# Kernel tuning notes

Measured on AMD Instinct MI355X. Metric: run time of the kernel, lower is better.

## Reference

```python
import jax, jax.numpy as jnp
import numpy as np

N, DIM = 20000, 2
E2, E3 = 150000, 100000
H = 512
IN_PAIR = 2 * DIM + 2    # arity*dim + arity (sigma repeated per object)
IN_TRIPLE = 3 * DIM + 3


def _lin(k, fan_in, fan_out):
    return jax.random.normal(k, (fan_in, fan_out), jnp.float32) / np.sqrt(fan_in)


def setup_inputs() -> dict:
    key = jax.random.key(0)
    ks = jax.random.split(key, 18)
    inp = {
        "x": jax.random.normal(ks[0], (N, DIM), jnp.float32),
        "sigma": jax.random.uniform(ks[1], (1,), jnp.float32) + 0.1,
        "edges_pair": jax.random.randint(ks[2], (E2, 2), 0, N),
        "edges_triple": jax.random.randint(ks[3], (E3, 3), 0, N),
        # per-relation-type TimeInputEnergyMLP params (2 hidden layers + scalar head)
        "pW1": _lin(ks[4], IN_PAIR, H), "pb1": jnp.zeros((H,), jnp.float32),
        "pW2": _lin(ks[5], H, H),       "pb2": jnp.zeros((H,), jnp.float32),
        "pW3": _lin(ks[6], H, 1),       "pb3": jnp.zeros((1,), jnp.float32),
        "tW1": _lin(ks[7], IN_TRIPLE, H), "tb1": jnp.zeros((H,), jnp.float32),
        "tW2": _lin(ks[8], H, H),         "tb2": jnp.zeros((H,), jnp.float32),
        "tW3": _lin(ks[9], H, 1),         "tb3": jnp.zeros((1,), jnp.float32),
    }
    return inp


def _mlp_energy(h, W1, b1, W2, b2, W3, b3):
    # h: (E, in_dim) -> (E, 1) scalar energy per edge
    h = jax.nn.silu(h @ W1 + b1)
    h = jax.nn.silu(h @ W2 + b2)
    return h @ W3 + b3


def reference(x, sigma, edges_pair, edges_triple,
              pW1, pb1, pW2, pb2, pW3, pb3,
              tW1, tb1, tW2, tb2, tW3, tb3):
    def total_energy(xx):
        # pair edges: gather -> (E2, 2*DIM), sigma repeated per object -> (E2, 2)
        xp = xx[edges_pair].reshape(edges_pair.shape[0], -1)
        sp = jnp.broadcast_to(sigma, (edges_pair.shape[0], 2))
        ep = _mlp_energy(jnp.concatenate([xp, sp], axis=-1),
                         pW1, pb1, pW2, pb2, pW3, pb3).sum()
        # triple edges
        xt = xx[edges_triple].reshape(edges_triple.shape[0], -1)
        st = jnp.broadcast_to(sigma, (edges_triple.shape[0], 3))
        et = _mlp_energy(jnp.concatenate([xt, st], axis=-1),
                         tW1, tb1, tW2, tb2, tW3, tb3).sum()
        return ep + et

    energy, grad = jax.value_and_grad(total_energy)(x)
    return energy, grad
```

## Files before the change

### kernel.cpp

```cpp
#include <hip/hip_runtime.h>
#include <hip/hip_bf16.h>

#define HDIM 512
#define TILE 64
#define TPB 512

typedef __attribute__((ext_vector_type(8))) short short8;
typedef __attribute__((ext_vector_type(4))) short s16x4;
typedef __attribute__((ext_vector_type(4))) float f32x4;

__device__ __forceinline__ unsigned short f2bf(float x) {
  __hip_bfloat16 h = __float2bfloat16(x);
  return *reinterpret_cast<unsigned short*>(&h);
}
__device__ __forceinline__ float bf2f(unsigned short h) {
  return __uint_as_float(((unsigned)h) << 16);
}
__device__ __forceinline__ float fsig(float z) {
  return __builtin_amdgcn_rcpf(1.f + __expf(-z));
}
__device__ __forceinline__ int bidx(int e, int n) {
  return e * HDIM + (n ^ ((e & 7) << 4));
}

__global__ void prep_weights(const float* __restrict__ pW2, const float* __restrict__ tW2,
                             unsigned short* __restrict__ pWf, unsigned short* __restrict__ pWb,
                             unsigned short* __restrict__ tWf, unsigned short* __restrict__ tWb) {
  int i = blockIdx.x * blockDim.x + threadIdx.x;
  if (i >= HDIM * HDIM) return;
  int j  = i & 7;
  int l  = (i >> 3) & 63;
  int kb = (i >> 9) & 15;
  int nb = i >> 13;
  int kpos = kb * 32 + ((l >> 4) << 3) + j;
  int npos = nb * 16 + (l & 15);
  pWf[i] = f2bf(pW2[kpos * HDIM + npos]);
  pWb[i] = f2bf(pW2[npos * HDIM + kpos]);
  tWf[i] = f2bf(tW2[kpos * HDIM + npos]);
  tWb[i] = f2bf(tW2[npos * HDIM + kpos]);
}

__global__ void prep_w1(const float* __restrict__ W1, int IN, int GD,
                        unsigned short* __restrict__ hi, unsigned short* __restrict__ lo,
                        unsigned short* __restrict__ p5) {
  int i = blockIdx.x * blockDim.x + threadIdx.x;
  if (i < 32 * 64 * 8) {
    int j = i & 7, l = (i >> 3) & 63, nb = i >> 9;
    int k = ((l >> 4) << 3) + j;
    int col = nb * 16 + (l & 15);
    float v = (k < IN) ? W1[k * HDIM + col] : 0.f;
    unsigned short h = f2bf(v);
    hi[i] = h;
    lo[i] = f2bf(v - bf2f(h));
  } else if (i < 32 * 64 * 8 + 16 * 64 * 8) {
    int i2 = i - 32 * 64 * 8;
    int j = i2 & 7, l = (i2 >> 3) & 63, kk = i2 >> 9;
    int lm = l & 15, q = l >> 4;
    int k = kk * 32 + q * 8 + j;
    p5[i2] = f2bf((lm < GD) ? W1[lm * HDIM + k] : 0.f);
  }
}

__global__ void __launch_bounds__(TPB, 2)
energy_kernel(const float* __restrict__ x, const float* __restrict__ sigp,
              const int* __restrict__ ep, const int* __restrict__ et,
              int E2, int E3, int nb2,
              const unsigned short* __restrict__ pW1hi, const unsigned short* __restrict__ pW1lo,
              const unsigned short* __restrict__ pW1p5,
              const unsigned short* __restrict__ tW1hi, const unsigned short* __restrict__ tW1lo,
              const unsigned short* __restrict__ tW1p5,
              const float* __restrict__ pb1, const float* __restrict__ tb1,
              const unsigned short* __restrict__ pWf, const unsigned short* __restrict__ pWb,
              const unsigned short* __restrict__ tWf, const unsigned short* __restrict__ tWb,
              const float* __restrict__ pb2, const float* __restrict__ tb2,
              const float* __restrict__ pw3, const float* __restrict__ tw3,
              const float* __restrict__ pb3, const float* __restrict__ tb3,
              float* __restrict__ out) {
  __shared__ __align__(16) unsigned short bufA[TILE * HDIM];
  __shared__ __align__(16) float h0s[TILE][16];
  __shared__ float dh0sT[8][TILE];
  __shared__ int   idxs[TILE * 3];
  __shared__ float blockE;

  const bool isP = (int)blockIdx.x < nb2;
  const int arity = isP ? 2 : 3;
  const int GD = 2 * arity;
  const int Etot = isP ? E2 : E3;
  const int* __restrict__ edges = isP ? ep : et;
  const unsigned short* __restrict__ W1hi = isP ? pW1hi : tW1hi;
  const unsigned short* __restrict__ W1lo = isP ? pW1lo : tW1lo;
  const unsigned short* __restrict__ W1p5 = isP ? pW1p5 : tW1p5;
  const unsigned short* __restrict__ Wf = isP ? pWf : tWf;
  const unsigned short* __restrict__ Wb = isP ? pWb : tWb;
  const float* __restrict__ b1 = isP ? pb1 : tb1;
  const float* __restrict__ b2 = isP ? pb2 : tb2;
  const float* __restrict__ w3 = isP ? pw3 : tw3;
  const float* __restrict__ b3p = isP ? pb3 : tb3;

  const int tid  = threadIdx.x;
  const int lane = tid & 63;
  const int w    = tid >> 6;
  const int q    = lane >> 4;
  const int lm   = lane & 15;
  const int tile0 = (isP ? (int)blockIdx.x : (int)blockIdx.x - nb2) * TILE;
  const int vcnt  = min(TILE, Etot - tile0);
  const float sigma = sigp[0];

  if (tid == 0) blockE = 0.f;
  ((float*)dh0sT)[tid] = 0.f;
  if (tid < TILE * arity) {
    int e = tid / arity;
    idxs[tid] = (e < vcnt) ? edges[(size_t)tile0 * arity + tid] : 0;
  }
  __syncthreads();
  if (tid < TILE) {
#pragma unroll
    for (int k = 0; k < 16; ++k) h0s[tid][k] = 0.f;
    if (tid < vcnt) {
      for (int o = 0; o < arity; ++o) {
        int id = idxs[tid * arity + o];
        h0s[tid][o * 2 + 0] = x[id * 2 + 0];
        h0s[tid][o * 2 + 1] = x[id * 2 + 1];
        h0s[tid][arity * 2 + o] = sigma;
      }
    }
  }
  __syncthreads();

  const int n0 = w * 64;

  short8 Hh[4], Hl[4];
#pragma unroll
  for (int ef = 0; ef < 4; ++ef) {
    f32x4 v0 = {0.f, 0.f, 0.f, 0.f}, v1 = {0.f, 0.f, 0.f, 0.f};
    if (q < 2) {
      const float* p = &h0s[ef * 16 + lm][q * 8];
      v0 = *(const f32x4*)p;
      v1 = *(const f32x4*)(p + 4);
    }
#pragma unroll
    for (int j = 0; j < 4; ++j) {
      unsigned short ha = f2bf(v0[j]);
      Hh[ef][j] = (short)ha;
      Hl[ef][j] = (short)f2bf(v0[j] - bf2f(ha));
      unsigned short hb = f2bf(v1[j]);
      Hh[ef][j + 4] = (short)hb;
      Hl[ef][j + 4] = (short)f2bf(v1[j] - bf2f(hb));
    }
  }

  f32x4 acc[4][4];
#pragma unroll
  for (int mf = 0; mf < 4; ++mf)
#pragma unroll
    for (int ef = 0; ef < 4; ++ef) acc[mf][ef] = (f32x4){0.f, 0.f, 0.f, 0.f};

#pragma unroll
  for (int mf = 0; mf < 4; ++mf) {
    short8 A1h = *(const short8*)(W1hi + (((w * 4 + mf) * 64 + lane) << 3));
    short8 A1l = *(const short8*)(W1lo + (((w * 4 + mf) * 64 + lane) << 3));
#pragma unroll
    for (int ef = 0; ef < 4; ++ef) {
      acc[mf][ef] = __builtin_amdgcn_mfma_f32_16x16x32_bf16(A1h, Hh[ef], acc[mf][ef], 0, 0, 0);
      acc[mf][ef] = __builtin_amdgcn_mfma_f32_16x16x32_bf16(A1l, Hh[ef], acc[mf][ef], 0, 0, 0);
      acc[mf][ef] = __builtin_amdgcn_mfma_f32_16x16x32_bf16(A1h, Hl[ef], acc[mf][ef], 0, 0, 0);
    }
  }
#pragma unroll
  for (int mf = 0; mf < 4; ++mf) {
    f32x4 b1x = *(const f32x4*)&b1[n0 + mf * 16 + q * 4];
#pragma unroll
    for (int ef = 0; ef < 4; ++ef) {
      bool val = (ef * 16 + lm) < vcnt;
      s16x4 pk;
#pragma unroll
      for (int r = 0; r < 4; ++r) {
        float z = acc[mf][ef][r] + b1x[r];
        float s = fsig(z);
        pk[r] = (short)f2bf(val ? z * s : 0.f);
      }
      *(s16x4*)&bufA[bidx(ef * 16 + lm, n0 + mf * 16 + q * 4)] = pk;
    }
  }
  __syncthreads();

#pragma unroll
  for (int mf = 0; mf < 4; ++mf)
#pragma unroll
    for (int ef = 0; ef < 4; ++ef) acc[mf][ef] = (f32x4){0.f, 0.f, 0.f, 0.f};

  {
    short8 af_cur[4];
#pragma unroll
    for (int mf = 0; mf < 4; ++mf)
      af_cur[mf] = *(const short8*)(Wf + ((((w * 4 + mf) * 16 + 0) * 64 + lane) << 3));
#pragma unroll
    for (int kk = 0; kk < 16; ++kk) {
      short8 af_nxt[4];
      if (kk < 15) {
#pragma unroll
        for (int mf = 0; mf < 4; ++mf)
          af_nxt[mf] = *(const short8*)(Wf + ((((w * 4 + mf) * 16 + kk + 1) * 64 + lane) << 3));
      }
      short8 hb[4];
#pragma unroll
      for (int ef = 0; ef < 4; ++ef)
        hb[ef] = *(const short8*)&bufA[bidx(ef * 16 + lm, kk * 32 + q * 8)];
      __builtin_amdgcn_s_setprio(1);
#pragma unroll
      for (int mf = 0; mf < 4; ++mf)
#pragma unroll
        for (int ef = 0; ef < 4; ++ef)
          acc[mf][ef] = __builtin_amdgcn_mfma_f32_16x16x32_bf16(af_cur[mf], hb[ef], acc[mf][ef], 0, 0, 0);
      __builtin_amdgcn_s_setprio(0);
#pragma unroll
      for (int mf = 0; mf < 4; ++mf) af_cur[mf] = af_nxt[mf];
    }
  }

  float epart = 0.f;
#pragma unroll
  for (int mf = 0; mf < 4; ++mf) {
    f32x4 b2x = *(const f32x4*)&b2[n0 + mf * 16 + q * 4];
    f32x4 w3x = *(const f32x4*)&w3[n0 + mf * 16 + q * 4];
#pragma unroll
    for (int ef = 0; ef < 4; ++ef) {
      bool val = (ef * 16 + lm) < vcnt;
#pragma unroll
      for (int r = 0; r < 4; ++r) {
        float z = acc[mf][ef][r] + b2x[r];
        float s = fsig(z);
        float h2 = z * s;
        float sp = s * (1.f + z * (1.f - s));
        epart += val ? h2 * w3x[r] : 0.f;
        acc[mf][ef][r] = val ? w3x[r] * sp : 0.f;
      }
    }
  }
#pragma unroll
  for (int off = 32; off > 0; off >>= 1) epart += __shfl_down(epart, off, 64);
  if (lane == 0) atomicAdd(&blockE, epart);

  __syncthreads();
#pragma unroll
  for (int mf = 0; mf < 4; ++mf)
#pragma unroll
    for (int ef = 0; ef < 4; ++ef) {
      s16x4 pk;
#pragma unroll
      for (int r = 0; r < 4; ++r) pk[r] = (short)f2bf(acc[mf][ef][r]);
      *(s16x4*)&bufA[bidx(ef * 16 + lm, n0 + mf * 16 + q * 4)] = pk;
    }
  __syncthreads();
  if (tid == 0) atomicAdd(out, blockE + (float)vcnt * b3p[0]);

#pragma unroll
  for (int mf = 0; mf < 4; ++mf)
#pragma unroll
    for (int ef = 0; ef < 4; ++ef) acc[mf][ef] = (f32x4){0.f, 0.f, 0.f, 0.f};

  {
    short8 af_cur[4];
#pragma unroll
    for (int mf = 0; mf < 4; ++mf)
      af_cur[mf] = *(const short8*)(Wb + ((((w * 4 + mf) * 16 + 0) * 64 + lane) << 3));
#pragma unroll
    for (int kk = 0; kk < 16; ++kk) {
      short8 af_nxt[4];
      if (kk < 15) {
#pragma unroll
        for (int mf = 0; mf < 4; ++mf)
          af_nxt[mf] = *(const short8*)(Wb + ((((w * 4 + mf) * 16 + kk + 1) * 64 + lane) << 3));
      }
      short8 hb[4];
#pragma unroll
      for (int ef = 0; ef < 4; ++ef)
        hb[ef] = *(const short8*)&bufA[bidx(ef * 16 + lm, kk * 32 + q * 8)];
      __builtin_amdgcn_s_setprio(1);
#pragma unroll
      for (int mf = 0; mf < 4; ++mf)
#pragma unroll
        for (int ef = 0; ef < 4; ++ef)
          acc[mf][ef] = __builtin_amdgcn_mfma_f32_16x16x32_bf16(af_cur[mf], hb[ef], acc[mf][ef], 0, 0, 0);
      __builtin_amdgcn_s_setprio(0);
#pragma unroll
      for (int mf = 0; mf < 4; ++mf) af_cur[mf] = af_nxt[mf];
    }
  }

#pragma unroll
  for (int mf = 0; mf < 4; ++mf) {
    short8 A1h = *(const short8*)(W1hi + (((w * 4 + mf) * 64 + lane) << 3));
    f32x4 zacc[4];
#pragma unroll
    for (int ef = 0; ef < 4; ++ef) zacc[ef] = (f32x4){0.f, 0.f, 0.f, 0.f};
#pragma unroll
    for (int ef = 0; ef < 4; ++ef)
      zacc[ef] = __builtin_amdgcn_mfma_f32_16x16x32_bf16(A1h, Hh[ef], zacc[ef], 0, 0, 0);
    f32x4 b1x = *(const f32x4*)&b1[n0 + mf * 16 + q * 4];
#pragma unroll
    for (int ef = 0; ef < 4; ++ef)
#pragma unroll
      for (int r = 0; r < 4; ++r) {
        float z = zacc[ef][r] + b1x[r];
        float s = fsig(z);
        float sp = s * (1.f + z * (1.f - s));
        acc[mf][ef][r] *= sp;
      }
  }
  __syncthreads();
#pragma unroll
  for (int mf = 0; mf < 4; ++mf)
#pragma unroll
    for (int ef = 0; ef < 4; ++ef) {
      s16x4 pk;
#pragma unroll
      for (int r = 0; r < 4; ++r) pk[r] = (short)f2bf(acc[mf][ef][r]);
      *(s16x4*)&bufA[bidx(ef * 16 + lm, n0 + mf * 16 + q * 4)] = pk;
    }
  __syncthreads();

  {
    f32x4 pacc[4];
#pragma unroll
    for (int ef = 0; ef < 4; ++ef) pacc[ef] = (f32x4){0.f, 0.f, 0.f, 0.f};
#pragma unroll
    for (int t = 0; t < 2; ++t) {
      int kk = w * 2 + t;
      short8 a5 = *(const short8*)(W1p5 + ((kk * 64 + lane) << 3));
      short8 db[4];
#pragma unroll
      for (int ef = 0; ef < 4; ++ef)
        db[ef] = *(const short8*)&bufA[bidx(ef * 16 + lm, kk * 32 + q * 8)];
#pragma unroll
      for (int ef = 0; ef < 4; ++ef)
        pacc[ef] = __builtin_amdgcn_mfma_f32_16x16x32_bf16(a5, db[ef], pacc[ef], 0, 0, 0);
    }
#pragma unroll
    for (int ef = 0; ef < 4; ++ef)
#pragma unroll
      for (int r = 0; r < 4; ++r) {
        int g = q * 4 + r;
        if (g < GD) atomicAdd(&dh0sT[g][ef * 16 + lm], pacc[ef][r]);
      }
  }
  __syncthreads();

  {
    int e = tid & 63, g = tid >> 6;
    if (e < vcnt && g < GD) {
      int obj = g >> 1, d = g & 1;
      atomicAdd(&out[1 + idxs[e * arity + obj] * 2 + d], dh0sT[g][e]);
    }
  }
}

extern "C" void kernel_launch(void* const* d_in, const int* in_sizes, int n_in,
                              void* d_out, int out_size, void* d_ws, size_t ws_size,
                              hipStream_t stream) {
  const float* x    = (const float*)d_in[0];
  const float* sig  = (const float*)d_in[1];
  const int*   ep   = (const int*)d_in[2];
  const int*   et   = (const int*)d_in[3];
  const float* pW1  = (const float*)d_in[4];
  const float* pb1  = (const float*)d_in[5];
  const float* pW2  = (const float*)d_in[6];
  const float* pb2  = (const float*)d_in[7];
  const float* pW3  = (const float*)d_in[8];
  const float* pb3  = (const float*)d_in[9];
  const float* tW1  = (const float*)d_in[10];
  const float* tb1  = (const float*)d_in[11];
  const float* tW2  = (const float*)d_in[12];
  const float* tb2  = (const float*)d_in[13];
  const float* tW3  = (const float*)d_in[14];
  const float* tb3  = (const float*)d_in[15];
  const int E2 = in_sizes[2] / 2;
  const int E3 = in_sizes[3] / 3;
  float* out = (float*)d_out;

  unsigned short* pWf = (unsigned short*)d_ws;
  unsigned short* pWb = pWf + HDIM * HDIM;
  unsigned short* tWf = pWb + HDIM * HDIM;
  unsigned short* tWb = tWf + HDIM * HDIM;
  unsigned short* pW1hi = tWb + HDIM * HDIM;
  unsigned short* pW1lo = pW1hi + 32 * 64 * 8;
  unsigned short* pW1p5 = pW1lo + 32 * 64 * 8;
  unsigned short* tW1hi = pW1p5 + 16 * 64 * 8;
  unsigned short* tW1lo = tW1hi + 32 * 64 * 8;
  unsigned short* tW1p5 = tW1lo + 32 * 64 * 8;

  const int nb2 = (E2 + TILE - 1) / TILE;
  const int nb3 = (E3 + TILE - 1) / TILE;

  hipMemsetAsync(d_out, 0, (size_t)out_size * sizeof(float), stream);
  prep_weights<<<(HDIM * HDIM + 255) / 256, 256, 0, stream>>>(pW2, tW2, pWf, pWb, tWf, tWb);
  prep_w1<<<(32 * 64 * 8 + 16 * 64 * 8 + 255) / 256, 256, 0, stream>>>(pW1, 6, 4, pW1hi, pW1lo, pW1p5);
  prep_w1<<<(32 * 64 * 8 + 16 * 64 * 8 + 255) / 256, 256, 0, stream>>>(tW1, 9, 6, tW1hi, tW1lo, tW1p5);
  energy_kernel<<<nb2 + nb3, TPB, 0, stream>>>(
      x, sig, ep, et, E2, E3, nb2,
      pW1hi, pW1lo, pW1p5, tW1hi, tW1lo, tW1p5, pb1, tb1,
      pWf, pWb, tWf, tWb, pb2, tb2, pW3, tW3, pb3, tb3, out);
}
```

Measured before the change: 436.8 us.

## Double edge tile to 128 with 1024-thread blocks and narrower per-wave column slices

Raises the edge tile from 64 to 128 and the block size from 512 to 1024 threads, so each of the 16 waves now owns 32 hidden columns across 8 edge fragments instead of 64 columns across 4. Each weight fragment loaded from global memory now feeds twice as many MFMAs, halving weight traffic per edge, and the per-block setup, barriers and atomics are spread over more edges. The backward recompute of layer-1 activations now rebuilds the bf16 inputs from shared memory instead of keeping them in registers. The larger block drops the two-blocks-per-CU launch bound and doubles the shared buffer, which may reduce occupancy and latency hiding.

```diff
diff --git a/kernel.cpp b/kernel.cpp
--- a/kernel.cpp
+++ b/kernel.cpp
@@ -2,8 +2,8 @@
 #include <hip/hip_bf16.h>
 
 #define HDIM 512
-#define TILE 64
-#define TPB 512
+#define TILE 128
+#define TPB 1024
 
 typedef __attribute__((ext_vector_type(8))) short short8;
 typedef __attribute__((ext_vector_type(4))) short s16x4;
@@ -61,7 +61,7 @@
   }
 }
 
-__global__ void __launch_bounds__(TPB, 2)
+__global__ void __launch_bounds__(TPB)
 energy_kernel(const float* __restrict__ x, const float* __restrict__ sigp,
               const int* __restrict__ ep, const int* __restrict__ et,
               int E2, int E3, int nb2,
@@ -127,50 +127,52 @@
   }
   __syncthreads();
 
-  const int n0 = w * 64;
-
-  short8 Hh[4], Hl[4];
-#pragma unroll
-  for (int ef = 0; ef < 4; ++ef) {
-    f32x4 v0 = {0.f, 0.f, 0.f, 0.f}, v1 = {0.f, 0.f, 0.f, 0.f};
-    if (q < 2) {
-      const float* p = &h0s[ef * 16 + lm][q * 8];
-      v0 = *(const f32x4*)p;
-      v1 = *(const f32x4*)(p + 4);
-    }
-#pragma unroll
-    for (int j = 0; j < 4; ++j) {
-      unsigned short ha = f2bf(v0[j]);
-      Hh[ef][j] = (short)ha;
-      Hl[ef][j] = (short)f2bf(v0[j] - bf2f(ha));
-      unsigned short hb = f2bf(v1[j]);
-      Hh[ef][j + 4] = (short)hb;
-      Hl[ef][j + 4] = (short)f2bf(v1[j] - bf2f(hb));
-    }
-  }
-
-  f32x4 acc[4][4];
-#pragma unroll
-  for (int mf = 0; mf < 4; ++mf)
-#pragma unroll
-    for (int ef = 0; ef < 4; ++ef) acc[mf][ef] = (f32x4){0.f, 0.f, 0.f, 0.f};
-
-#pragma unroll
-  for (int mf = 0; mf < 4; ++mf) {
-    short8 A1h = *(const short8*)(W1hi + (((w * 4 + mf) * 64 + lane) << 3));
-    short8 A1l = *(const short8*)(W1lo + (((w * 4 + mf) * 64 + lane) << 3));
-#pragma unroll
-    for (int ef = 0; ef < 4; ++ef) {
-      acc[mf][ef] = __builtin_amdgcn_mfma_f32_16x16x32_bf16(A1h, Hh[ef], acc[mf][ef], 0, 0, 0);
-      acc[mf][ef] = __builtin_amdgcn_mfma_f32_16x16x32_bf16(A1l, Hh[ef], acc[mf][ef], 0, 0, 0);
-      acc[mf][ef] = __builtin_amdgcn_mfma_f32_16x16x32_bf16(A1h, Hl[ef], acc[mf][ef], 0, 0, 0);
-    }
-  }
-#pragma unroll
-  for (int mf = 0; mf < 4; ++mf) {
+  const int n0 = w * 32;
+
+  f32x4 acc[2][8];
+#pragma unroll
+  for (int mf = 0; mf < 2; ++mf)
+#pragma unroll
+    for (int ef = 0; ef < 8; ++ef) acc[mf][ef] = (f32x4){0.f, 0.f, 0.f, 0.f};
+
+#pragma unroll
+  for (int h = 0; h < 2; ++h) {
+    short8 Hh[4], Hl[4];
+#pragma unroll
+    for (int e4 = 0; e4 < 4; ++e4) {
+      f32x4 v0 = {0.f, 0.f, 0.f, 0.f}, v1 = {0.f, 0.f, 0.f, 0.f};
+      if (q < 2) {
+        const float* p = &h0s[(h * 4 + e4) * 16 + lm][q * 8];
+        v0 = *(const f32x4*)p;
+        v1 = *(const f32x4*)(p + 4);
+      }
+#pragma unroll
+      for (int j = 0; j < 4; ++j) {
+        unsigned short ha = f2bf(v0[j]);
+        Hh[e4][j] = (short)ha;
+        Hl[e4][j] = (short)f2bf(v0[j] - bf2f(ha));
+        unsigned short hb = f2bf(v1[j]);
+        Hh[e4][j + 4] = (short)hb;
+        Hl[e4][j + 4] = (short)f2bf(v1[j] - bf2f(hb));
+      }
+    }
+#pragma unroll
+    for (int mf = 0; mf < 2; ++mf) {
+      short8 A1h = *(const short8*)(W1hi + (((w * 2 + mf) * 64 + lane) << 3));
+      short8 A1l = *(const short8*)(W1lo + (((w * 2 + mf) * 64 + lane) << 3));
+#pragma unroll
+      for (int e4 = 0; e4 < 4; ++e4) {
+        acc[mf][h * 4 + e4] = __builtin_amdgcn_mfma_f32_16x16x32_bf16(A1h, Hh[e4], acc[mf][h * 4 + e4], 0, 0, 0);
+        acc[mf][h * 4 + e4] = __builtin_amdgcn_mfma_f32_16x16x32_bf16(A1l, Hh[e4], acc[mf][h * 4 + e4], 0, 0, 0);
+        acc[mf][h * 4 + e4] = __builtin_amdgcn_mfma_f32_16x16x32_bf16(A1h, Hl[e4], acc[mf][h * 4 + e4], 0, 0, 0);
+      }
+    }
+  }
+#pragma unroll
+  for (int mf = 0; mf < 2; ++mf) {
     f32x4 b1x = *(const f32x4*)&b1[n0 + mf * 16 + q * 4];
 #pragma unroll
-    for (int ef = 0; ef < 4; ++ef) {
+    for (int ef = 0; ef < 8; ++ef) {
       bool val = (ef * 16 + lm) < vcnt;
       s16x4 pk;
 #pragma unroll
@@ -185,46 +187,46 @@
   __syncthreads();
 
 #pragma unroll
-  for (int mf = 0; mf < 4; ++mf)
-#pragma unroll
-    for (int ef = 0; ef < 4; ++ef) acc[mf][ef] = (f32x4){0.f, 0.f, 0.f, 0.f};
+  for (int mf = 0; mf < 2; ++mf)
+#pragma unroll
+    for (int ef = 0; ef < 8; ++ef) acc[mf][ef] = (f32x4){0.f, 0.f, 0.f, 0.f};
 
   {
-    short8 af_cur[4];
-#pragma unroll
-    for (int mf = 0; mf < 4; ++mf)
-      af_cur[mf] = *(const short8*)(Wf + ((((w * 4 + mf) * 16 + 0) * 64 + lane) << 3));
+    short8 af_cur[2];
+#pragma unroll
+    for (int mf = 0; mf < 2; ++mf)
+      af_cur[mf] = *(const short8*)(Wf + ((((w * 2 + mf) * 16 + 0) * 64 + lane) << 3));
 #pragma unroll
     for (int kk = 0; kk < 16; ++kk) {
-      short8 af_nxt[4];
+      short8 af_nxt[2];
       if (kk < 15) {
 #pragma unroll
-        for (int mf = 0; mf < 4; ++mf)
-          af_nxt[mf] = *(const short8*)(Wf + ((((w * 4 + mf) * 16 + kk + 1) * 64 + lane) << 3));
-      }
-      short8 hb[4];
-#pragma unroll
-      for (int ef = 0; ef < 4; ++ef)
+        for (int mf = 0; mf < 2; ++mf)
+          af_nxt[mf] = *(const short8*)(Wf + ((((w * 2 + mf) * 16 + kk + 1) * 64 + lane) << 3));
+      }
+      short8 hb[8];
+#pragma unroll
+      for (int ef = 0; ef < 8; ++ef)
         hb[ef] = *(const short8*)&bufA[bidx(ef * 16 + lm, kk * 32 + q * 8)];
       __builtin_amdgcn_s_setprio(1);
 #pragma unroll
-      for (int mf = 0; mf < 4; ++mf)
-#pragma unroll
-        for (int ef = 0; ef < 4; ++ef)
+      for (int mf = 0; mf < 2; ++mf)
+#pragma unroll
+        for (int ef = 0; ef < 8; ++ef)
           acc[mf][ef] = __builtin_amdgcn_mfma_f32_16x16x32_bf16(af_cur[mf], hb[ef], acc[mf][ef], 0, 0, 0);
       __builtin_amdgcn_s_setprio(0);
 #pragma unroll
-      for (int mf = 0; mf < 4; ++mf) af_cur[mf] = af_nxt[mf];
+      for (int mf = 0; mf < 2; ++mf) af_cur[mf] = af_nxt[mf];
     }
   }
 
   float epart = 0.f;
 #pragma unroll
-  for (int mf = 0; mf < 4; ++mf) {
+  for (int mf = 0; mf < 2; ++mf) {
     f32x4 b2x = *(const f32x4*)&b2[n0 + mf * 16 + q * 4];
     f32x4 w3x = *(const f32x4*)&w3[n0 + mf * 16 + q * 4];
 #pragma unroll
-    for (int ef = 0; ef < 4; ++ef) {
+    for (int ef = 0; ef < 8; ++ef) {
       bool val = (ef * 16 + lm) < vcnt;
 #pragma unroll
       for (int r = 0; r < 4; ++r) {
@@ -243,9 +245,9 @@
 
   __syncthreads();
 #pragma unroll
-  for (int mf = 0; mf < 4; ++mf)
-#pragma unroll
-    for (int ef = 0; ef < 4; ++ef) {
+  for (int mf = 0; mf < 2; ++mf)
+#pragma unroll
+    for (int ef = 0; ef < 8; ++ef) {
       s16x4 pk;
 #pragma unroll
       for (int r = 0; r < 4; ++r) pk[r] = (short)f2bf(acc[mf][ef][r]);
@@ -255,64 +257,82 @@
   if (tid == 0) atomicAdd(out, blockE + (float)vcnt * b3p[0]);
 
 #pragma unroll
-  for (int mf = 0; mf < 4; ++mf)
-#pragma unroll
-    for (int ef = 0; ef < 4; ++ef) acc[mf][ef] = (f32x4){0.f, 0.f, 0.f, 0.f};
+  for (int mf = 0; mf < 2; ++mf)
+#pragma unroll
+    for (int ef = 0; ef < 8; ++ef) acc[mf][ef] = (f32x4){0.f, 0.f, 0.f, 0.f};
 
   {
-    short8 af_cur[4];
-#pragma unroll
-    for (int mf = 0; mf < 4; ++mf)
-      af_cur[mf] = *(const short8*)(Wb + ((((w * 4 + mf) * 16 + 0) * 64 + lane) << 3));
+    short8 af_cur[2];
+#pragma unroll
+    for (int mf = 0; mf < 2; ++mf)
+      af_cur[mf] = *(const short8*)(Wb + ((((w * 2 + mf) * 16 + 0) * 64 + lane) << 3));
 #pragma unroll
     for (int kk = 0; kk < 16; ++kk) {
-      short8 af_nxt[4];
+      short8 af_nxt[2];
       if (kk < 15) {
 #pragma unroll
-        for (int mf = 0; mf < 4; ++mf)
-          af_nxt[mf] = *(const short8*)(Wb + ((((w * 4 + mf) * 16 + kk + 1) * 64 + lane) << 3));
-      }
-      short8 hb[4];
-#pragma unroll
-      for (int ef = 0; ef < 4; ++ef)
+        for (int mf = 0; mf < 2; ++mf)
+          af_nxt[mf] = *(const short8*)(Wb + ((((w * 2 + mf) * 16 + kk + 1) * 64 + lane) << 3));
+      }
+      short8 hb[8];
+#pragma unroll
+      for (int ef = 0; ef < 8; ++ef)
         hb[ef] = *(const short8*)&bufA[bidx(ef * 16 + lm, kk * 32 + q * 8)];
       __builtin_amdgcn_s_setprio(1);
 #pragma unroll
-      for (int mf = 0; mf < 4; ++mf)
-#pragma unroll
-        for (int ef = 0; ef < 4; ++ef)
+      for (int mf = 0; mf < 2; ++mf)
+#pragma unroll
+        for (int ef = 0; ef < 8; ++ef)
           acc[mf][ef] = __builtin_amdgcn_mfma_f32_16x16x32_bf16(af_cur[mf], hb[ef], acc[mf][ef], 0, 0, 0);
       __builtin_amdgcn_s_setprio(0);
 #pragma unroll
-      for (int mf = 0; mf < 4; ++mf) af_cur[mf] = af_nxt[mf];
-    }
-  }
-
-#pragma unroll
-  for (int mf = 0; mf < 4; ++mf) {
-    short8 A1h = *(const short8*)(W1hi + (((w * 4 + mf) * 64 + lane) << 3));
-    f32x4 zacc[4];
-#pragma unroll
-    for (int ef = 0; ef < 4; ++ef) zacc[ef] = (f32x4){0.f, 0.f, 0.f, 0.f};
-#pragma unroll
-    for (int ef = 0; ef < 4; ++ef)
-      zacc[ef] = __builtin_amdgcn_mfma_f32_16x16x32_bf16(A1h, Hh[ef], zacc[ef], 0, 0, 0);
-    f32x4 b1x = *(const f32x4*)&b1[n0 + mf * 16 + q * 4];
-#pragma unroll
-    for (int ef = 0; ef < 4; ++ef)
-#pragma unroll
-      for (int r = 0; r < 4; ++r) {
-        float z = zacc[ef][r] + b1x[r];
-        float s = fsig(z);
-        float sp = s * (1.f + z * (1.f - s));
-        acc[mf][ef][r] *= sp;
-      }
-  }
-  __syncthreads();
-#pragma unroll
-  for (int mf = 0; mf < 4; ++mf)
-#pragma unroll
-    for (int ef = 0; ef < 4; ++ef) {
+      for (int mf = 0; mf < 2; ++mf) af_cur[mf] = af_nxt[mf];
+    }
+  }
+
+  {
+    short8 A1h[2];
+#pragma unroll
+    for (int mf = 0; mf < 2; ++mf)
+      A1h[mf] = *(const short8*)(W1hi + (((w * 2 + mf) * 64 + lane) << 3));
+    f32x4 b1x[2];
+#pragma unroll
+    for (int mf = 0; mf < 2; ++mf) b1x[mf] = *(const f32x4*)&b1[n0 + mf * 16 + q * 4];
+#pragma unroll
+    for (int ef = 0; ef < 8; ++ef) {
+      short8 Hh;
+      {
+        f32x4 v0 = {0.f, 0.f, 0.f, 0.f}, v1 = {0.f, 0.f, 0.f, 0.f};
+        if (q < 2) {
+          const float* p = &h0s[ef * 16 + lm][q * 8];
+          v0 = *(const f32x4*)p;
+          v1 = *(const f32x4*)(p + 4);
+        }
+#pragma unroll
+        for (int j = 0; j < 4; ++j) {
+          Hh[j] = (short)f2bf(v0[j]);
+          Hh[j + 4] = (short)f2bf(v1[j]);
+        }
+      }
+#pragma unroll
+      for (int mf = 0; mf < 2; ++mf) {
+        f32x4 zacc = (f32x4){0.f, 0.f, 0.f, 0.f};
+        zacc = __builtin_amdgcn_mfma_f32_16x16x32_bf16(A1h[mf], Hh, zacc, 0, 0, 0);
+#pragma unroll
+        for (int r = 0; r < 4; ++r) {
+          float z = zacc[r] + b1x[mf][r];
+          float s = fsig(z);
+          float sp = s * (1.f + z * (1.f - s));
+          acc[mf][ef][r] *= sp;
+        }
+      }
+    }
+  }
+  __syncthreads();
+#pragma unroll
+  for (int mf = 0; mf < 2; ++mf)
+#pragma unroll
+    for (int ef = 0; ef < 8; ++ef) {
       s16x4 pk;
 #pragma unroll
       for (int r = 0; r < 4; ++r) pk[r] = (short)f2bf(acc[mf][ef][r]);
@@ -321,23 +341,18 @@
   __syncthreads();
 
   {
-    f32x4 pacc[4];
-#pragma unroll
-    for (int ef = 0; ef < 4; ++ef) pacc[ef] = (f32x4){0.f, 0.f, 0.f, 0.f};
-#pragma unroll
-    for (int t = 0; t < 2; ++t) {
-      int kk = w * 2 + t;
-      short8 a5 = *(const short8*)(W1p5 + ((kk * 64 + lane) << 3));
-      short8 db[4];
-#pragma unroll
-      for (int ef = 0; ef < 4; ++ef)
-        db[ef] = *(const short8*)&bufA[bidx(ef * 16 + lm, kk * 32 + q * 8)];
-#pragma unroll
-      for (int ef = 0; ef < 4; ++ef)
-        pacc[ef] = __builtin_amdgcn_mfma_f32_16x16x32_bf16(a5, db[ef], pacc[ef], 0, 0, 0);
-    }
-#pragma unroll
-    for (int ef = 0; ef < 4; ++ef)
+    const int kk = w;
+    short8 a5 = *(const short8*)(W1p5 + ((kk * 64 + lane) << 3));
+    f32x4 pacc[8];
+#pragma unroll
+    for (int ef = 0; ef < 8; ++ef) pacc[ef] = (f32x4){0.f, 0.f, 0.f, 0.f};
+#pragma unroll
+    for (int ef = 0; ef < 8; ++ef) {
+      short8 db = *(const short8*)&bufA[bidx(ef * 16 + lm, kk * 32 + q * 8)];
+      pacc[ef] = __builtin_amdgcn_mfma_f32_16x16x32_bf16(a5, db, pacc[ef], 0, 0, 0);
+    }
+#pragma unroll
+    for (int ef = 0; ef < 8; ++ef)
 #pragma unroll
       for (int r = 0; r < 4; ++r) {
         int g = q * 4 + r;
@@ -347,7 +362,7 @@
   __syncthreads();
 
   {
-    int e = tid & 63, g = tid >> 6;
+    int e = tid & 127, g = tid >> 7;
     if (e < vcnt && g < GD) {
       int obj = g >> 1, d = g & 1;
       atomicAdd(&out[1 + idxs[e * arity + obj] * 2 + d], dh0sT[g][e]);
```

Measured after the change: 863.2 us. 97.6% more time.
